# Optimization experiments

Measured on AMD Instinct MI355X. Metric: run time of the kernel, lower is better.

The kernel has to match this reference:

```python
import jax, jax.numpy as jnp
import numpy as np

TOP_K = 2


def setup_inputs() -> dict:
    key = jax.random.key(0)
    kx, kw = jax.random.split(key)
    x = jax.random.normal(kx, (4, 4096, 2048), dtype=jnp.float32)
    router_weights = jax.random.normal(kw, (8, 2048), dtype=jnp.float32) * 0.02
    return {"x": x, "router_weights": router_weights}


def reference(x, router_weights):
    # logits[b,s,e] = sum_d x[b,s,d] * W[e,d]
    logits = jnp.einsum('bsd,ed->bse', x, router_weights)
    # top-k over experts, then softmax over the selected k logits
    top_vals, top_idx = jax.lax.top_k(logits, TOP_K)  # [B,S,K]
    gates = jax.nn.softmax(top_vals, axis=-1)
    indices = top_idx.astype(jnp.int32)
    return indices, gates, logits
```

## Files before the change

### kernel.cpp

```cpp
#include <hip/hip_runtime.h>
#include <math.h>


constexpr int D      = 2048;
constexpr int E      = 8;
constexpr int T      = 8;
constexpr int WAVES  = 4;
constexpr int TOKENS = 16384;

__device__ __forceinline__ bool better(float va, int ia, float vb, int ib) {
    return (va > vb) || (va == vb && ia < ib);
}

__global__ __launch_bounds__(256, 2)
void moe_router_kernel(const float* __restrict__ x,
                       const float* __restrict__ w,
                       float* __restrict__ out)
{
    __shared__ float scr[WAVES][64][64];

    const int lane = threadIdx.x & 63;
    const int wave = threadIdx.x >> 6;
    const int tok0 = (blockIdx.x * WAVES + wave) * T;

    float acc[T * E];
#pragma unroll
    for (int i = 0; i < T * E; ++i) acc[i] = 0.0f;

#pragma unroll 1
    for (int it = 0; it < D / 256; ++it) {
        const int d = it * 256 + lane * 4;
        float4 xv[T];
#pragma unroll
        for (int t = 0; t < T; ++t)
            xv[t] = *reinterpret_cast<const float4*>(x + (size_t)(tok0 + t) * D + d);
        float4 wv[E];
#pragma unroll
        for (int e = 0; e < E; ++e)
            wv[e] = *reinterpret_cast<const float4*>(w + e * D + d);
#pragma unroll
        for (int t = 0; t < T; ++t) {
#pragma unroll
            for (int e = 0; e < E; ++e) {
                float a = acc[t * E + e];
                a = fmaf(xv[t].x, wv[e].x, a);
                a = fmaf(xv[t].y, wv[e].y, a);
                a = fmaf(xv[t].z, wv[e].z, a);
                a = fmaf(xv[t].w, wv[e].w, a);
                acc[t * E + e] = a;
            }
        }
    }

#pragma unroll
    for (int p = 0; p < 64; ++p)
        scr[wave][p][(lane + p) & 63] = acc[p];

    __syncthreads();

    float s0 = 0.f, s1 = 0.f, s2 = 0.f, s3 = 0.f;
#pragma unroll
    for (int j = 0; j < 64; j += 4) {
        s0 += scr[wave][lane][(lane + j + 0) & 63];
        s1 += scr[wave][lane][(lane + j + 1) & 63];
        s2 += scr[wave][lane][(lane + j + 2) & 63];
        s3 += scr[wave][lane][(lane + j + 3) & 63];
    }
    const float logit = (s0 + s1) + (s2 + s3);

    const int t     = lane >> 3;
    const int e     = lane & 7;
    const int token = tok0 + t;

    float* out_idx    = out;
    float* out_gate   = out + TOKENS * 2;
    float* out_logits = out + TOKENS * 4;

    out_logits[(size_t)token * E + e] = logit;

    float v1 = logit, v2 = -INFINITY;
    int   i1 = e,     i2 = E;
#pragma unroll
    for (int m = 1; m <= 4; m <<= 1) {
        float ov1 = __shfl_xor(v1, m, 64);
        int   oi1 = __shfl_xor(i1, m, 64);
        float ov2 = __shfl_xor(v2, m, 64);
        int   oi2 = __shfl_xor(i2, m, 64);
        float nv1, nv2; int ni1, ni2;
        if (better(v1, i1, ov1, oi1)) {
            nv1 = v1; ni1 = i1;
            if (better(v2, i2, ov1, oi1)) { nv2 = v2;  ni2 = i2;  }
            else                          { nv2 = ov1; ni2 = oi1; }
        } else {
            nv1 = ov1; ni1 = oi1;
            if (better(ov2, oi2, v1, i1)) { nv2 = ov2; ni2 = oi2; }
            else                          { nv2 = v1;  ni2 = i1;  }
        }
        v1 = nv1; i1 = ni1; v2 = nv2; i2 = ni2;
    }

    if (e < 2) {
        const float ed  = expf(v2 - v1);
        const float inv = 1.0f / (1.0f + ed);
        const float g   = (e == 0) ? inv : ed * inv;
        out_idx [token * 2 + e] = (float)((e == 0) ? i1 : i2);
        out_gate[token * 2 + e] = g;
    }
}

extern "C" void kernel_launch(void* const* d_in, const int* in_sizes, int n_in,
                              void* d_out, int out_size, void* d_ws, size_t ws_size,
                              hipStream_t stream) {
    const float* x = (const float*)d_in[0];
    const float* w = (const float*)d_in[1];
    float* out = (float*)d_out;
    hipLaunchKernelGGL(moe_router_kernel, dim3(512), dim3(256), 0, stream,
                       x, w, out);
}
```

Measured before the change: 193.1 us.

## Stage router weights in LDS and double-buffer x loads in registers

The 64KB router weight matrix is copied into shared memory once per block, reusing the existing scratch buffer, and then read from LDS instead of global memory. The main loop is unrolled by two and register-double-buffered, so the next chunk of x is loaded while the current chunk is being multiplied. This is meant to hide global load latency on the memory-bound x stream. The cost is higher register pressure from the two x buffers, plus an extra barrier before the scratch space is reused.

```diff
diff --git a/kernel.cpp b/kernel.cpp
--- a/kernel.cpp
+++ b/kernel.cpp
@@ -17,54 +17,99 @@
                        const float* __restrict__ w,
                        float* __restrict__ out)
 {
-    __shared__ float scr[WAVES][64][64];
+    __shared__ float smem[WAVES * 64 * 64];
 
-    const int lane = threadIdx.x & 63;
-    const int wave = threadIdx.x >> 6;
+    const int tid  = threadIdx.x;
+    const int lane = tid & 63;
+    const int wave = tid >> 6;
     const int tok0 = (blockIdx.x * WAVES + wave) * T;
+
+#pragma unroll
+    for (int i = 0; i < 16; ++i) {
+        reinterpret_cast<float4*>(smem)[i * 256 + tid] =
+            reinterpret_cast<const float4*>(w)[i * 256 + tid];
+    }
 
     float acc[T * E];
 #pragma unroll
     for (int i = 0; i < T * E; ++i) acc[i] = 0.0f;
 
+    const float* xrow = x + (size_t)tok0 * D + lane * 4;
+
+    float4 xA[T], xB[T];
+#pragma unroll
+    for (int t = 0; t < T; ++t)
+        xA[t] = *reinterpret_cast<const float4*>(xrow + (size_t)t * D);
+
+    __syncthreads();
+
 #pragma unroll 1
-    for (int it = 0; it < D / 256; ++it) {
-        const int d = it * 256 + lane * 4;
-        float4 xv[T];
+    for (int it = 0; it < D / 256; it += 2) {
 #pragma unroll
         for (int t = 0; t < T; ++t)
-            xv[t] = *reinterpret_cast<const float4*>(x + (size_t)(tok0 + t) * D + d);
-        float4 wv[E];
+            xB[t] = *reinterpret_cast<const float4*>(xrow + (size_t)t * D + (it + 1) * 256);
+
+        {
+            float4 wv[E];
 #pragma unroll
-        for (int e = 0; e < E; ++e)
-            wv[e] = *reinterpret_cast<const float4*>(w + e * D + d);
+            for (int e = 0; e < E; ++e)
+                wv[e] = *reinterpret_cast<const float4*>(&smem[e * D + it * 256 + lane * 4]);
 #pragma unroll
-        for (int t = 0; t < T; ++t) {
+            for (int t = 0; t < T; ++t) {
 #pragma unroll
-            for (int e = 0; e < E; ++e) {
-                float a = acc[t * E + e];
-                a = fmaf(xv[t].x, wv[e].x, a);
-                a = fmaf(xv[t].y, wv[e].y, a);
-                a = fmaf(xv[t].z, wv[e].z, a);
-                a = fmaf(xv[t].w, wv[e].w, a);
-                acc[t * E + e] = a;
+                for (int e = 0; e < E; ++e) {
+                    float a = acc[t * E + e];
+                    a = fmaf(xA[t].x, wv[e].x, a);
+                    a = fmaf(xA[t].y, wv[e].y, a);
+                    a = fmaf(xA[t].z, wv[e].z, a);
+                    a = fmaf(xA[t].w, wv[e].w, a);
+                    acc[t * E + e] = a;
+                }
+            }
+        }
+
+        if (it + 2 < D / 256) {
+#pragma unroll
+            for (int t = 0; t < T; ++t)
+                xA[t] = *reinterpret_cast<const float4*>(xrow + (size_t)t * D + (it + 2) * 256);
+        }
+
+        {
+            float4 wv[E];
+#pragma unroll
+            for (int e = 0; e < E; ++e)
+                wv[e] = *reinterpret_cast<const float4*>(&smem[e * D + (it + 1) * 256 + lane * 4]);
+#pragma unroll
+            for (int t = 0; t < T; ++t) {
+#pragma unroll
+                for (int e = 0; e < E; ++e) {
+                    float a = acc[t * E + e];
+                    a = fmaf(xB[t].x, wv[e].x, a);
+                    a = fmaf(xB[t].y, wv[e].y, a);
+                    a = fmaf(xB[t].z, wv[e].z, a);
+                    a = fmaf(xB[t].w, wv[e].w, a);
+                    acc[t * E + e] = a;
+                }
             }
         }
     }
 
+    __syncthreads();
+
+    float* scr = smem + wave * 64 * 64;
 #pragma unroll
     for (int p = 0; p < 64; ++p)
-        scr[wave][p][(lane + p) & 63] = acc[p];
+        scr[p * 64 + ((lane + p) & 63)] = acc[p];
 
     __syncthreads();
 
     float s0 = 0.f, s1 = 0.f, s2 = 0.f, s3 = 0.f;
 #pragma unroll
     for (int j = 0; j < 64; j += 4) {
-        s0 += scr[wave][lane][(lane + j + 0) & 63];
-        s1 += scr[wave][lane][(lane + j + 1) & 63];
-        s2 += scr[wave][lane][(lane + j + 2) & 63];
-        s3 += scr[wave][lane][(lane + j + 3) & 63];
+        s0 += scr[lane * 64 + ((lane + j + 0) & 63)];
+        s1 += scr[lane * 64 + ((lane + j + 1) & 63)];
+        s2 += scr[lane * 64 + ((lane + j + 2) & 63)];
+        s3 += scr[lane * 64 + ((lane + j + 3) & 63)];
     }
     const float logit = (s0 + s1) + (s2 + s3);
 
```

Measured after the change: 191.8 us. No clear change (-0.7%).
